# Kernel tuning notes

Hardware: AMD Instinct MI355X
Metric: run time of the kernel (lower is better)

Reference implementation:

```python
import jax, jax.numpy as jnp
import numpy as np

N_NODES = 100000
N_EDGES = 1600000
IN_DIM = 192   # n_shapes(64) * n_dims(3)
H1, H2 = 64, 32


def _glorot(key, shape):
    lim = np.sqrt(6.0 / (shape[0] + shape[1])).astype(np.float32)
    return jax.random.uniform(key, shape, jnp.float32, -lim, lim)


def setup_inputs() -> dict:
    key = jax.random.key(0)
    ks = jax.random.split(key, 8)
    verts = jax.random.normal(ks[0], (N_NODES, IN_DIM), jnp.float32)
    edges = jax.random.randint(ks[1], (N_EDGES, 2), 0, N_NODES)
    return {
        "verts": verts,
        "edges": edges,
        "W0_1": _glorot(ks[2], (IN_DIM, H1)),
        "W1_1": _glorot(ks[3], (IN_DIM, H1)),
        "b1": jnp.zeros((H1,), jnp.float32),
        "W0_2": _glorot(ks[4], (H1, H2)),
        "W1_2": _glorot(ks[5], (H1, H2)),
        "b2": jnp.zeros((H2,), jnp.float32),
    }


def cheb_conv(x, src, dst, W0, W1, b, n):
    # ChebConv K=2 with lambda_max=2: L_hat = -D^{-1/2} A D^{-1/2} (zero diagonal)
    deg = jax.ops.segment_sum(jnp.ones(src.shape, x.dtype), src, num_segments=n)
    d_inv = jnp.where(deg > 0, jax.lax.rsqrt(jnp.maximum(deg, 1.0)), 0.0)
    norm = -d_inv[src] * d_inv[dst]                      # [E]
    Tx1 = jax.ops.segment_sum(norm[:, None] * x[src], dst, num_segments=n)  # [n,F]
    return x @ W0 + Tx1 @ W1 + b


def reference(verts, edges, W0_1, W1_1, b1, W0_2, W1_2, b2):
    n = verts.shape[0]
    src, dst = edges[:, 0], edges[:, 1]  # edge_index rows after edges.t()
    x = jax.nn.relu(cheb_conv(verts, src, dst, W0_1, W1_1, b1, n))
    return cheb_conv(x, src, dst, W0_2, W1_2, b2, n)
```

## Files before the change

kernel.cpp:

```cpp
#include <hip/hip_runtime.h>

#define N_NODES 100000
#define N_EDGES 1600000
#define IN_DIM  192
#define H1      64
#define H2      32
#define NBKT    391
#define CAP_D   4608
#define NP1     782
#define NG      1563
#define K1GRID  2345

typedef __attribute__((ext_vector_type(8))) short short8;
typedef __attribute__((ext_vector_type(4))) float f32x4;

__device__ inline short f2bf(float f) {
    union { float f; unsigned u; } v; v.f = f;
    unsigned r = (v.u + 0x7FFFu + ((v.u >> 16) & 1u)) >> 16;
    return (short)r;
}
__device__ inline float bf2f(unsigned short s) {
    union { unsigned u; float f; } v; v.u = ((unsigned)s) << 16;
    return v.f;
}

__global__ __launch_bounds__(512) void init_kernel(int* __restrict__ bucket_next) {
    int b = threadIdx.x;
    if (b < 512) bucket_next[b] = b * CAP_D;
}

__global__ __launch_bounds__(256) void prep_w_kernel(
    const float* __restrict__ W0_1, const float* __restrict__ W1_1,
    const float* __restrict__ W0_2, const float* __restrict__ W1_2,
    short* __restrict__ Bt1, short* __restrict__ Bt2) {
    int idx = blockIdx.x * 256 + threadIdx.x;
    if (idx < 128 * IN_DIM) {
        int n = idx / IN_DIM, k = idx % IN_DIM;
        float v = (n < H1) ? W0_1[(size_t)k * H1 + n] : W1_1[(size_t)k * H1 + (n - H1)];
        Bt1[idx] = f2bf(v);
    } else {
        int j = idx - 128 * IN_DIM;
        if (j < 64 * H1) {
            int n = j / H1, k = j % H1;
            float v = (n < H2) ? W0_2[(size_t)k * H2 + n] : W1_2[(size_t)k * H2 + (n - H2)];
            Bt2[j] = f2bf(v);
        }
    }
}

__global__ __launch_bounds__(256) void k1_fused(
    const int* __restrict__ edges, int* __restrict__ degi, int* __restrict__ bucket_next,
    int* __restrict__ bins,
    const float* __restrict__ verts, const short* __restrict__ Bt1,
    const float* __restrict__ b1, float* __restrict__ h, short* __restrict__ y1b) {
    __shared__ int cnt_l[512];
    __shared__ int cur_l[512];
    int b = blockIdx.x;
    int tid = threadIdx.x;
    if (b % 3 == 0) {
        int p = b / 3;
        cnt_l[tid] = 0; cnt_l[tid + 256] = 0;
        __syncthreads();
        int ebase = p * 2048 + tid * 8;
        int2 ed[8]; int bkt[8];
#pragma unroll
        for (int i = 0; i < 8; ++i) {
            int e = ebase + i;
            if (e < N_EDGES) {
                ed[i] = ((const int2*)edges)[e];
                bkt[i] = ed[i].y >> 8;
                atomicAdd(&cnt_l[bkt[i]], 1);
            } else bkt[i] = -1;
        }
        __syncthreads();
        {
            int c0 = cnt_l[tid];
            cur_l[tid] = (c0 > 0) ? atomicAdd(&bucket_next[tid], c0) : 0;
            int c1 = cnt_l[tid + 256];
            cur_l[tid + 256] = (c1 > 0) ? atomicAdd(&bucket_next[tid + 256], c1) : 0;
        }
        __syncthreads();
#pragma unroll
        for (int i = 0; i < 8; ++i) {
            if (bkt[i] >= 0) {
                int slot = atomicAdd(&cur_l[bkt[i]], 1);
                if (slot < (bkt[i] + 1) * CAP_D)
                    bins[slot] = ((ed[i].y & 255) << 17) | ed[i].x;
                atomicAdd(&degi[ed[i].x], 1);
            }
        }
        return;
    }
    int g = b - b / 3 - 1;
    int lane = tid & 63;
    int wave = tid >> 6;
    int rowbase = g * 64 + wave * 16;
    int lr = lane & 15;
    int lk = (lane >> 4) * 8;

    int row = rowbase + lr;
    int rc = (row < N_NODES) ? row : (N_NODES - 1);
    const float* p = verts + (size_t)rc * IN_DIM + lk;
    short8 a[6];
#pragma unroll
    for (int ks = 0; ks < 6; ++ks) {
        f32x4 u0 = *(const f32x4*)(p + ks * 32);
        f32x4 u1 = *(const f32x4*)(p + ks * 32 + 4);
        short8 t;
        t[0] = f2bf(u0[0]); t[1] = f2bf(u0[1]); t[2] = f2bf(u0[2]); t[3] = f2bf(u0[3]);
        t[4] = f2bf(u1[0]); t[5] = f2bf(u1[1]); t[6] = f2bf(u1[2]); t[7] = f2bf(u1[3]);
        a[ks] = t;
    }

    f32x4 acc[8] = {};
#pragma unroll
    for (int cf = 0; cf < 8; ++cf) {
        const short* bp = Bt1 + (size_t)(cf * 16 + lr) * IN_DIM + lk;
#pragma unroll
        for (int ks = 0; ks < 6; ++ks) {
            short8 bb = *(const short8*)(bp + ks * 32);
            acc[cf] = __builtin_amdgcn_mfma_f32_16x16x32_bf16(a[ks], bb, acc[cf], 0, 0, 0);
        }
    }

    int srow = (lane >> 4) * 4;
#pragma unroll
    for (int cf = 0; cf < 8; ++cf) {
        int colc = cf * 16 + lr;
        float bias = (colc < H1) ? b1[colc] : 0.f;
#pragma unroll
        for (int r = 0; r < 4; ++r) {
            int orow = rowbase + srow + r;
            if (orow < N_NODES) {
                float v = acc[cf][r];
                if (colc < H1) h[(size_t)orow * H1 + colc] = v + bias;
                else           y1b[(size_t)orow * H1 + (colc - H1)] = f2bf(v);
            }
        }
    }
}

__global__ __launch_bounds__(256) void csr_kernel(
    const int* __restrict__ bins, const int* __restrict__ bucket_next,
    const int* __restrict__ degi, float* __restrict__ dinv,
    int* __restrict__ row_beg, int* __restrict__ row_end, int* __restrict__ col) {
    __shared__ int cnt_l[256];
    __shared__ int seg_l[256];
    __shared__ int s[256];
    int b = blockIdx.x;
    int tid = threadIdx.x;
    int beg = b * CAP_D;
    int fill = bucket_next[b] - beg;
    if (fill > CAP_D) fill = CAP_D;
    cnt_l[tid] = 0;
    __syncthreads();
    for (int i = tid; i < fill; i += 256)
        atomicAdd(&cnt_l[bins[beg + i] >> 17], 1);
    __syncthreads();
    int v = cnt_l[tid];
    s[tid] = v;
    __syncthreads();
    for (int off = 1; off < 256; off <<= 1) {
        int t = (tid >= off) ? s[tid - off] : 0;
        __syncthreads();
        s[tid] += t;
        __syncthreads();
    }
    int excl = s[tid] - v;
    seg_l[tid] = beg + excl;
    int n = b * 256 + tid;
    if (n < N_NODES) {
        row_beg[n] = beg + excl;
        row_end[n] = beg + excl + v;
        int d = degi[n];
        dinv[n] = (d > 0) ? rsqrtf((float)d) : 0.f;
    }
    __syncthreads();
    for (int i = tid; i < fill; i += 256) {
        int w = bins[beg + i];
        int slot = atomicAdd(&seg_l[w >> 17], 1);
        col[slot] = w & 0x1FFFF;
    }
}

__global__ __launch_bounds__(256) void gather1_kernel(
    const int* __restrict__ row_beg, const int* __restrict__ row_end,
    const int* __restrict__ col, const float* __restrict__ dinv,
    const float* __restrict__ h, const unsigned short* __restrict__ y1b,
    short* __restrict__ hb) {
    int n = blockIdx.x * 4 + (threadIdx.x >> 6);
    if (n >= N_NODES) return;
    int lane = threadIdx.x & 63;
    int beg = row_beg[n], end = row_end[n];
    float acc = 0.f;
    int i = beg;
    for (; i + 4 <= end; i += 4) {
        int s0 = col[i], s1 = col[i + 1], s2 = col[i + 2], s3 = col[i + 3];
        float w0 = dinv[s0], w1 = dinv[s1], w2 = dinv[s2], w3 = dinv[s3];
        float v0 = bf2f(y1b[(size_t)s0 * H1 + lane]);
        float v1 = bf2f(y1b[(size_t)s1 * H1 + lane]);
        float v2 = bf2f(y1b[(size_t)s2 * H1 + lane]);
        float v3 = bf2f(y1b[(size_t)s3 * H1 + lane]);
        acc += w0 * v0 + w1 * v1 + w2 * v2 + w3 * v3;
    }
    for (; i < end; ++i) {
        int sc = col[i];
        acc += dinv[sc] * bf2f(y1b[(size_t)sc * H1 + lane]);
    }
    size_t idx = (size_t)n * H1 + lane;
    float hf = h[idx] - dinv[n] * acc;
    hb[idx] = f2bf(fmaxf(hf, 0.f));
}

__global__ __launch_bounds__(256) void gemm2_mfma(
    const short* __restrict__ hb, const short* __restrict__ Bt2,
    const float* __restrict__ b2, float* __restrict__ out, short* __restrict__ y2b) {
    int lane = threadIdx.x & 63;
    int wave = threadIdx.x >> 6;
    int rowbase = blockIdx.x * 128 + wave * 32;
    int lr = lane & 15;
    int lk = (lane >> 4) * 8;

    short8 a[2][2];
#pragma unroll
    for (int mr = 0; mr < 2; ++mr) {
        int row = rowbase + mr * 16 + lr;
        int rc = (row < N_NODES) ? row : (N_NODES - 1);
        const short* p = hb + (size_t)rc * H1 + lk;
        a[mr][0] = *(const short8*)(p);
        a[mr][1] = *(const short8*)(p + 32);
    }

    f32x4 acc[2][4] = {};
#pragma unroll
    for (int cf = 0; cf < 4; ++cf) {
        const short* bp = Bt2 + (size_t)(cf * 16 + lr) * H1 + lk;
#pragma unroll
        for (int ks = 0; ks < 2; ++ks) {
            short8 b = *(const short8*)(bp + ks * 32);
            acc[0][cf] = __builtin_amdgcn_mfma_f32_16x16x32_bf16(a[0][ks], b, acc[0][cf], 0, 0, 0);
            acc[1][cf] = __builtin_amdgcn_mfma_f32_16x16x32_bf16(a[1][ks], b, acc[1][cf], 0, 0, 0);
        }
    }

    int srow = (lane >> 4) * 4;
#pragma unroll
    for (int mr = 0; mr < 2; ++mr) {
#pragma unroll
        for (int cf = 0; cf < 4; ++cf) {
            int colc = cf * 16 + lr;
            float bias = (colc < H2) ? b2[colc] : 0.f;
#pragma unroll
            for (int r = 0; r < 4; ++r) {
                int row = rowbase + mr * 16 + srow + r;
                if (row < N_NODES) {
                    float v = acc[mr][cf][r];
                    if (colc < H2) out[(size_t)row * H2 + colc] = v + bias;
                    else           y2b[(size_t)row * H2 + (colc - H2)] = f2bf(v);
                }
            }
        }
    }
}

__global__ __launch_bounds__(256) void gather2_kernel(
    const int* __restrict__ row_beg, const int* __restrict__ row_end,
    const int* __restrict__ col, const float* __restrict__ dinv,
    const unsigned short* __restrict__ y2b, float* __restrict__ out) {
    int wave = (blockIdx.x * 256 + threadIdx.x) >> 6;
    int lane = threadIdx.x & 63;
    int n = wave * 2 + (lane >> 5);
    if (n >= N_NODES) return;
    int c32 = lane & 31;
    int beg = row_beg[n], end = row_end[n];
    float acc = 0.f;
    int i = beg;
    for (; i + 4 <= end; i += 4) {
        int s0 = col[i], s1 = col[i + 1], s2 = col[i + 2], s3 = col[i + 3];
        float w0 = dinv[s0], w1 = dinv[s1], w2 = dinv[s2], w3 = dinv[s3];
        float v0 = bf2f(y2b[(size_t)s0 * H2 + c32]);
        float v1 = bf2f(y2b[(size_t)s1 * H2 + c32]);
        float v2 = bf2f(y2b[(size_t)s2 * H2 + c32]);
        float v3 = bf2f(y2b[(size_t)s3 * H2 + c32]);
        acc += w0 * v0 + w1 * v1 + w2 * v2 + w3 * v3;
    }
    for (; i < end; ++i) {
        int sc = col[i];
        acc += dinv[sc] * bf2f(y2b[(size_t)sc * H2 + c32]);
    }
    size_t idx = (size_t)n * H2 + c32;
    out[idx] = out[idx] - dinv[n] * acc;
}

extern "C" void kernel_launch(void* const* d_in, const int* in_sizes, int n_in,
                              void* d_out, int out_size, void* d_ws, size_t ws_size,
                              hipStream_t stream) {
    const float* verts = (const float*)d_in[0];
    const int*   edges = (const int*)  d_in[1];
    const float* W0_1  = (const float*)d_in[2];
    const float* W1_1  = (const float*)d_in[3];
    const float* b1    = (const float*)d_in[4];
    const float* W0_2  = (const float*)d_in[5];
    const float* W1_2  = (const float*)d_in[6];
    const float* b2    = (const float*)d_in[7];
    float* out = (float*)d_out;

    char* ws = (char*)d_ws;
    auto align256 = [](size_t x) { return (x + 255) & ~(size_t)255; };
    size_t o = 0;
    auto alloc = [&](size_t bytes) { size_t r = o; o = align256(o + bytes); return r; };

    int*   degi        = (int*)  (ws + alloc((size_t)N_NODES * 4));
    int*   bucket_next = (int*)  (ws + alloc((size_t)512 * 4));
    int*   bins        = (int*)  (ws + alloc((size_t)NBKT * CAP_D * 4));
    int*   col         = (int*)  (ws + alloc((size_t)NBKT * CAP_D * 4));
    int*   row_beg     = (int*)  (ws + alloc((size_t)N_NODES * 4));
    int*   row_end     = (int*)  (ws + alloc((size_t)N_NODES * 4));
    float* dinv        = (float*)(ws + alloc((size_t)N_NODES * 4));
    short* Bt1         = (short*)(ws + alloc((size_t)128 * IN_DIM * 2));
    short* Bt2         = (short*)(ws + alloc((size_t)64 * H1 * 2));
    float* h           = (float*)(ws + alloc((size_t)N_NODES * H1 * 4));
    short* y1b         = (short*)(ws + alloc((size_t)N_NODES * H1 * 2));
    short* hb          = (short*)(ws + alloc((size_t)N_NODES * H1 * 2));
    short* y2b         = (short*)(ws + alloc((size_t)N_NODES * H2 * 2));

    hipMemsetAsync(degi, 0, (size_t)N_NODES * 4, stream);
    init_kernel  <<<1, 512, 0, stream>>>(bucket_next);
    prep_w_kernel<<<(128 * IN_DIM + 64 * H1 + 255) / 256, 256, 0, stream>>>(W0_1, W1_1, W0_2, W1_2, Bt1, Bt2);

    k1_fused  <<<K1GRID, 256, 0, stream>>>(edges, degi, bucket_next, bins, verts, Bt1, b1, h, y1b);
    csr_kernel<<<NBKT, 256, 0, stream>>>(bins, bucket_next, degi, dinv, row_beg, row_end, col);

    gather1_kernel<<<(N_NODES + 3) / 4, 256, 0, stream>>>(row_beg, row_end, col, dinv, h, (const unsigned short*)y1b, hb);
    gemm2_mfma    <<<(N_NODES + 127) / 128, 256, 0, stream>>>(hb, Bt2, b2, out, y2b);
    gather2_kernel<<<(N_NODES + 7) / 8, 256, 0, stream>>>(row_beg, row_end, col, dinv, (const unsigned short*)y2b, out);
}
```

Measured before the change: 245.2 us.

## Compute source degrees via byte-sized source buckets and store base term as bf16

Replaces the global per-edge atomicAdd on the degree array with a second bucketing pass. Each edge's low source byte goes into a per-256-node byte bucket, and the CSR kernel counts these in shared memory to get the degree. This removes 1.6M scattered global atomics and the memset of the degree array. Separately, the x@W0+b intermediate is now stored as bf16 instead of fp32 to halve its traffic, at some precision cost.

```diff
diff --git a/kernel.cpp b/kernel.cpp
--- a/kernel.cpp
+++ b/kernel.cpp
@@ -24,9 +24,9 @@
     return v.f;
 }
 
-__global__ __launch_bounds__(512) void init_kernel(int* __restrict__ bucket_next) {
-    int b = threadIdx.x;
-    if (b < 512) bucket_next[b] = b * CAP_D;
+__global__ __launch_bounds__(1024) void init_kernel(int* __restrict__ bucket_next) {
+    int i = threadIdx.x;
+    bucket_next[i] = (i & 511) * CAP_D;
 }
 
 __global__ __launch_bounds__(256) void prep_w_kernel(
@@ -49,44 +49,52 @@
 }
 
 __global__ __launch_bounds__(256) void k1_fused(
-    const int* __restrict__ edges, int* __restrict__ degi, int* __restrict__ bucket_next,
-    int* __restrict__ bins,
+    const int* __restrict__ edges, int* __restrict__ bucket_next,
+    int* __restrict__ bins_dst, unsigned char* __restrict__ bins_src,
     const float* __restrict__ verts, const short* __restrict__ Bt1,
-    const float* __restrict__ b1, float* __restrict__ h, short* __restrict__ y1b) {
-    __shared__ int cnt_l[512];
-    __shared__ int cur_l[512];
+    const float* __restrict__ b1, short* __restrict__ hbase, short* __restrict__ y1b) {
+    __shared__ int cntd[512];
+    __shared__ int curd[512];
+    __shared__ int cnts[512];
+    __shared__ int curs[512];
     int b = blockIdx.x;
     int tid = threadIdx.x;
     if (b % 3 == 0) {
         int p = b / 3;
-        cnt_l[tid] = 0; cnt_l[tid + 256] = 0;
+        cntd[tid] = 0; cntd[tid + 256] = 0;
+        cnts[tid] = 0; cnts[tid + 256] = 0;
         __syncthreads();
         int ebase = p * 2048 + tid * 8;
-        int2 ed[8]; int bkt[8];
+        int2 ed[8]; int bd[8], bs[8];
 #pragma unroll
         for (int i = 0; i < 8; ++i) {
             int e = ebase + i;
             if (e < N_EDGES) {
                 ed[i] = ((const int2*)edges)[e];
-                bkt[i] = ed[i].y >> 8;
-                atomicAdd(&cnt_l[bkt[i]], 1);
-            } else bkt[i] = -1;
+                bd[i] = ed[i].y >> 8;
+                bs[i] = ed[i].x >> 8;
+                atomicAdd(&cntd[bd[i]], 1);
+                atomicAdd(&cnts[bs[i]], 1);
+            } else { bd[i] = -1; bs[i] = -1; }
         }
         __syncthreads();
         {
-            int c0 = cnt_l[tid];
-            cur_l[tid] = (c0 > 0) ? atomicAdd(&bucket_next[tid], c0) : 0;
-            int c1 = cnt_l[tid + 256];
-            cur_l[tid + 256] = (c1 > 0) ? atomicAdd(&bucket_next[tid + 256], c1) : 0;
+            int c;
+            c = cntd[tid];       curd[tid]       = (c > 0) ? atomicAdd(&bucket_next[tid], c) : 0;
+            c = cntd[tid + 256]; curd[tid + 256] = (c > 0) ? atomicAdd(&bucket_next[tid + 256], c) : 0;
+            c = cnts[tid];       curs[tid]       = (c > 0) ? atomicAdd(&bucket_next[512 + tid], c) : 0;
+            c = cnts[tid + 256]; curs[tid + 256] = (c > 0) ? atomicAdd(&bucket_next[512 + tid + 256], c) : 0;
         }
         __syncthreads();
 #pragma unroll
         for (int i = 0; i < 8; ++i) {
-            if (bkt[i] >= 0) {
-                int slot = atomicAdd(&cur_l[bkt[i]], 1);
-                if (slot < (bkt[i] + 1) * CAP_D)
-                    bins[slot] = ((ed[i].y & 255) << 17) | ed[i].x;
-                atomicAdd(&degi[ed[i].x], 1);
+            if (bd[i] >= 0) {
+                int sd = atomicAdd(&curd[bd[i]], 1);
+                if (sd < (bd[i] + 1) * CAP_D)
+                    bins_dst[sd] = ((ed[i].y & 255) << 17) | ed[i].x;
+                int ss = atomicAdd(&curs[bs[i]], 1);
+                if (ss < (bs[i] + 1) * CAP_D)
+                    bins_src[ss] = (unsigned char)(ed[i].x & 255);
             }
         }
         return;
@@ -133,7 +141,7 @@
             int orow = rowbase + srow + r;
             if (orow < N_NODES) {
                 float v = acc[cf][r];
-                if (colc < H1) h[(size_t)orow * H1 + colc] = v + bias;
+                if (colc < H1) hbase[(size_t)orow * H1 + colc] = f2bf(v + bias);
                 else           y1b[(size_t)orow * H1 + (colc - H1)] = f2bf(v);
             }
         }
@@ -141,21 +149,27 @@
 }
 
 __global__ __launch_bounds__(256) void csr_kernel(
-    const int* __restrict__ bins, const int* __restrict__ bucket_next,
-    const int* __restrict__ degi, float* __restrict__ dinv,
+    const int* __restrict__ bins_dst, const unsigned char* __restrict__ bins_src,
+    const int* __restrict__ bucket_next, float* __restrict__ dinv,
     int* __restrict__ row_beg, int* __restrict__ row_end, int* __restrict__ col) {
     __shared__ int cnt_l[256];
     __shared__ int seg_l[256];
     __shared__ int s[256];
+    __shared__ int dcnt[256];
     int b = blockIdx.x;
     int tid = threadIdx.x;
     int beg = b * CAP_D;
-    int fill = bucket_next[b] - beg;
-    if (fill > CAP_D) fill = CAP_D;
+    int filld = bucket_next[b] - beg;
+    if (filld > CAP_D) filld = CAP_D;
+    int fills = bucket_next[512 + b] - beg;
+    if (fills > CAP_D) fills = CAP_D;
     cnt_l[tid] = 0;
+    dcnt[tid] = 0;
     __syncthreads();
-    for (int i = tid; i < fill; i += 256)
-        atomicAdd(&cnt_l[bins[beg + i] >> 17], 1);
+    for (int i = tid; i < filld; i += 256)
+        atomicAdd(&cnt_l[bins_dst[beg + i] >> 17], 1);
+    for (int i = tid; i < fills; i += 256)
+        atomicAdd(&dcnt[bins_src[beg + i]], 1);
     __syncthreads();
     int v = cnt_l[tid];
     s[tid] = v;
@@ -172,12 +186,12 @@
     if (n < N_NODES) {
         row_beg[n] = beg + excl;
         row_end[n] = beg + excl + v;
-        int d = degi[n];
+        int d = dcnt[tid];
         dinv[n] = (d > 0) ? rsqrtf((float)d) : 0.f;
     }
     __syncthreads();
-    for (int i = tid; i < fill; i += 256) {
-        int w = bins[beg + i];
+    for (int i = tid; i < filld; i += 256) {
+        int w = bins_dst[beg + i];
         int slot = atomicAdd(&seg_l[w >> 17], 1);
         col[slot] = w & 0x1FFFF;
     }
@@ -186,7 +200,7 @@
 __global__ __launch_bounds__(256) void gather1_kernel(
     const int* __restrict__ row_beg, const int* __restrict__ row_end,
     const int* __restrict__ col, const float* __restrict__ dinv,
-    const float* __restrict__ h, const unsigned short* __restrict__ y1b,
+    const unsigned short* __restrict__ hbase, const unsigned short* __restrict__ y1b,
     short* __restrict__ hb) {
     int n = blockIdx.x * 4 + (threadIdx.x >> 6);
     if (n >= N_NODES) return;
@@ -208,7 +222,7 @@
         acc += dinv[sc] * bf2f(y1b[(size_t)sc * H1 + lane]);
     }
     size_t idx = (size_t)n * H1 + lane;
-    float hf = h[idx] - dinv[n] * acc;
+    float hf = bf2f(hbase[idx]) - dinv[n] * acc;
     hb[idx] = f2bf(fmaxf(hf, 0.f));
 }
 
@@ -310,28 +324,32 @@
     size_t o = 0;
     auto alloc = [&](size_t bytes) { size_t r = o; o = align256(o + bytes); return r; };
 
-    int*   degi        = (int*)  (ws + alloc((size_t)N_NODES * 4));
-    int*   bucket_next = (int*)  (ws + alloc((size_t)512 * 4));
-    int*   bins        = (int*)  (ws + alloc((size_t)NBKT * CAP_D * 4));
+    int*   bucket_next = (int*)  (ws + alloc((size_t)1024 * 4));
+    int*   bins_dst    = (int*)  (ws + alloc((size_t)NBKT * CAP_D * 4));
+    unsigned char* bins_src = (unsigned char*)(ws + alloc((size_t)NBKT * CAP_D));
     int*   col         = (int*)  (ws + alloc((size_t)NBKT * CAP_D * 4));
     int*   row_beg     = (int*)  (ws + alloc((size_t)N_NODES * 4));
     int*   row_end     = (int*)  (ws + alloc((size_t)N_NODES * 4));
     float* dinv        = (float*)(ws + alloc((size_t)N_NODES * 4));
     short* Bt1         = (short*)(ws + alloc((size_t)128 * IN_DIM * 2));
     short* Bt2         = (short*)(ws + alloc((size_t)64 * H1 * 2));
-    float* h           = (float*)(ws + alloc((size_t)N_NODES * H1 * 4));
+    short* hbase       = (short*)(ws + alloc((size_t)N_NODES * H1 * 2));
     short* y1b         = (short*)(ws + alloc((size_t)N_NODES * H1 * 2));
     short* hb          = (short*)(ws + alloc((size_t)N_NODES * H1 * 2));
     short* y2b         = (short*)(ws + alloc((size_t)N_NODES * H2 * 2));
 
-    hipMemsetAsync(degi, 0, (size_t)N_NODES * 4, stream);
-    init_kernel  <<<1, 512, 0, stream>>>(bucket_next);
+    init_kernel  <<<1, 1024, 0, stream>>>(bucket_next);
     prep_w_kernel<<<(128 * IN_DIM + 64 * H1 + 255) / 256, 256, 0, stream>>>(W0_1, W1_1, W0_2, W1_2, Bt1, Bt2);
 
-    k1_fused  <<<K1GRID, 256, 0, stream>>>(edges, degi, bucket_next, bins, verts, Bt1, b1, h, y1b);
-    csr_kernel<<<NBKT, 256, 0, stream>>>(bins, bucket_next, degi, dinv, row_beg, row_end, col);
-
-    gather1_kernel<<<(N_NODES + 3) / 4, 256, 0, stream>>>(row_beg, row_end, col, dinv, h, (const unsigned short*)y1b, hb);
+    k1_fused  <<<K1GRID, 256, 0, stream>>>(edges, bucket_next, bins_dst, bins_src,
+                                           verts, Bt1, b1, hbase, y1b);
+    csr_kernel<<<NBKT, 256, 0, stream>>>(bins_dst, bins_src, bucket_next, dinv,
+                                         row_beg, row_end, col);
+
+    gather1_kernel<<<(N_NODES + 3) / 4, 256, 0, stream>>>(row_beg, row_end, col, dinv,
+                                                          (const unsigned short*)hbase,
+                                                          (const unsigned short*)y1b, hb);
     gemm2_mfma    <<<(N_NODES + 127) / 128, 256, 0, stream>>>(hb, Bt2, b2, out, y2b);
-    gather2_kernel<<<(N_NODES + 7) / 8, 256, 0, stream>>>(row_beg, row_end, col, dinv, (const unsigned short*)y2b, out);
-}
+    gather2_kernel<<<(N_NODES + 7) / 8, 256, 0, stream>>>(row_beg, row_end, col, dinv,
+                                                          (const unsigned short*)y2b, out);
+}
```

Measured after the change: 220.2 us. 10.2% less time.
